# Optimization experiments

Hardware: AMD Instinct MI355X
Metric: run time of the kernel (lower is better)

The kernel has to match this reference:

```python
import jax, jax.numpy as jnp
import numpy as np

T, D, N, K, H = 4096, 2560, 8, 4, 256
QUERY_PRE_ATTN_SCALAR = 256.0
ROPE_THETA = 10000.0
RMS_EPS = 1e-6
SLIDING_WINDOW = 1024
NEG_INF = -1e30


def setup_inputs() -> dict:
    key = jax.random.key(0)
    ks = jax.random.split(key, 6)
    return {
        "x": jax.random.normal(ks[0], (T, D), dtype=jnp.float32),
        "wq": jax.random.normal(ks[1], (D, N, H), dtype=jnp.float32) * 0.02,
        "wk": jax.random.normal(ks[2], (D, K, H), dtype=jnp.float32) * 0.02,
        "wv": jax.random.normal(ks[3], (D, K, H), dtype=jnp.float32) * 0.02,
        "wo": jax.random.normal(ks[4], (N, H, D), dtype=jnp.float32) * 0.02,
        "q_norm_w": jnp.ones((H,), dtype=jnp.float32),
        "k_norm_w": jnp.ones((H,), dtype=jnp.float32),
        "positions": jnp.arange(T, dtype=jnp.int32),
    }


def rms_norm(x, w, eps=RMS_EPS):
    rms = jnp.sqrt(jnp.mean(x * x, axis=-1, keepdims=True) + eps)
    return w * (x / rms)


def apply_rope(x, positions, head_dim, theta):
    # x: [T, heads, H]; rotate-half RoPE
    half = head_dim // 2
    inv_freq = theta ** (-(jnp.arange(half, dtype=jnp.float32) * 2.0 / head_dim))
    ang = positions.astype(jnp.float32)[:, None] * inv_freq  # [T, half]
    sin = jnp.sin(ang)[:, None, :]
    cos = jnp.cos(ang)[:, None, :]
    x1, x2 = jnp.split(x, 2, axis=-1)
    return jnp.concatenate([x1 * cos - x2 * sin, x2 * cos + x1 * sin], axis=-1)


def reference(x, wq, wk, wv, wo, q_norm_w, k_norm_w, positions):
    # QKV projections (per-head)
    q = jnp.einsum('td,dnh->tnh', x, wq)            # [T, N, H]
    q = rms_norm(q, q_norm_w)
    q = q * (QUERY_PRE_ATTN_SCALAR ** -0.5)
    q = apply_rope(q, positions, H, ROPE_THETA)

    k = jnp.einsum('td,dkh->tkh', x, wk)            # [T, K, H]
    k = rms_norm(k, k_norm_w)
    k = apply_rope(k, positions, H, ROPE_THETA)

    v = jnp.einsum('td,dkh->tkh', x, wv)            # [T, K, H]

    # GQA sliding-window causal attention
    G = N // K
    qh = q.reshape(T, K, G, H)
    scores = jnp.einsum('tkgh,skh->kgts', qh, k)    # [K, G, T, T]
    pq = positions[:, None]
    pk = positions[None, :]
    mask = (pk <= pq) & (pq - pk < SLIDING_WINDOW)  # [T, T]
    scores = jnp.where(mask, scores, NEG_INF)
    p = jax.nn.softmax(scores, axis=-1)
    attn = jnp.einsum('kgts,skh->tkgh', p, v).reshape(T, N, H)

    o = jnp.einsum('tnh,nhd->td', attn, wo)         # [T, D]
    new_kv_cache = jnp.stack([k, v])                # [2, T, K, H]
    return new_kv_cache, o
```

## Files before the change

### kernel.cpp

```cpp
#include <hip/hip_runtime.h>
#include <stdint.h>

#define T_TOK 4096
#define DM    2560
#define NQ    8
#define NKV   4
#define HD    256
#define WIN   1024

using bf16x8 = __attribute__((ext_vector_type(8))) short;
using f32x4  = __attribute__((ext_vector_type(4))) float;
typedef unsigned short u16;

__device__ __forceinline__ u16 f2bf(float x) {
  union { float f; uint32_t u; } v; v.f = x;
  uint32_t u = v.u;
  return (u16)((u + 0x7fffu + ((u >> 16) & 1u)) >> 16);
}
__device__ __forceinline__ float bf2f(u16 b) {
  union { uint32_t u; float f; } v; v.u = ((uint32_t)b) << 16;
  return v.f;
}

__device__ __forceinline__ void async_cp16(const void* g, void* lds) {
  __builtin_amdgcn_global_load_lds(
      (const __attribute__((address_space(1))) uint32_t*)(uintptr_t)g,
      (__attribute__((address_space(3))) uint32_t*)(uint32_t)(uintptr_t)lds,
      16, 0, 0);
}

__global__ __launch_bounds__(256) void convert_f32_bf16(
    const float* __restrict__ in, u16* __restrict__ out, int n)
{
  for (int i = (blockIdx.x * 256 + threadIdx.x) * 4; i < n; i += gridDim.x * 256 * 4) {
    float4 v = *(const float4*)(in + i);
    ushort4 o;
    o.x = f2bf(v.x); o.y = f2bf(v.y); o.z = f2bf(v.z); o.w = f2bf(v.w);
    *(ushort4*)(out + i) = o;
  }
}

__global__ __launch_bounds__(256) void transpose_f32_bf16(
    const float* __restrict__ in, u16* __restrict__ out, int R, int C)
{
  __shared__ u16 tile[64][65];
  const int r0 = blockIdx.y * 64, c0 = blockIdx.x * 64;
  const int tr = threadIdx.x >> 6, tc = threadIdx.x & 63;
  #pragma unroll
  for (int i = 0; i < 16; ++i) {
    int r = tr + i * 4;
    tile[r][tc] = f2bf(in[(size_t)(r0 + r) * C + c0 + tc]);
  }
  __syncthreads();
  #pragma unroll
  for (int i = 0; i < 16; ++i) {
    int c = tr + i * 4;
    out[(size_t)(c0 + c) * R + r0 + tc] = tile[tc][c];
  }
}

template<bool F32OUT>
__global__ __launch_bounds__(512, 2) void gemm256(
    const u16* __restrict__ A, const u16* __restrict__ B, void* __restrict__ Cv,
    int Kd, int lda, int ldb, int ldc)
{
  __shared__ __align__(16) u16 lds[2][2][256 * 64];
  const int tid = threadIdx.x;
  const int wave = tid >> 6, lane = tid & 63;
  const int lg = lane >> 4, lc = lane & 15;
  const int wr = wave >> 2, wc = wave & 3;
  const int m0 = blockIdx.y * 256, n0 = blockIdx.x * 256;
  const int NT = Kd >> 6;

  const int srow = tid >> 3;
  const int scol = ((tid & 7) * 16) ^ ((srow & 7) << 4);
  const u16* Ag = A + (size_t)(m0 + srow) * lda + (scol >> 1);
  const u16* Bg = B + (size_t)(n0 + srow) * ldb + (scol >> 1);
  char* ldsA0 = (char*)&lds[0][0][0];
  char* ldsB0 = (char*)&lds[0][1][0];
  char* ldsA1 = (char*)&lds[1][0][0];
  char* ldsB1 = (char*)&lds[1][1][0];

  #define STAGE256(LA, LB, KT) do {                                         \
    const int kc_ = (KT) * 64;                                              \
    _Pragma("unroll")                                                       \
    for (int li = 0; li < 4; ++li)                                          \
      async_cp16(Ag + (size_t)(li * 64) * lda + kc_, (LA) + li * 8192 + wave * 1024); \
    _Pragma("unroll")                                                       \
    for (int li = 0; li < 4; ++li)                                          \
      async_cp16(Bg + (size_t)(li * 64) * ldb + kc_, (LB) + li * 8192 + wave * 1024); \
  } while (0)

  const f32x4 zf = {0.f, 0.f, 0.f, 0.f};
  f32x4 acc[8][4];
  #pragma unroll
  for (int i = 0; i < 8; ++i)
    #pragma unroll
    for (int j = 0; j < 4; ++j) acc[i][j] = zf;

  STAGE256(ldsA0, ldsB0, 0);
  STAGE256(ldsA1, ldsB1, 1);
  asm volatile("s_waitcnt vmcnt(8)" ::: "memory");
  __builtin_amdgcn_s_barrier();
  __builtin_amdgcn_sched_barrier(0);

  for (int t = 0; t < NT; ++t) {
    const int cur = t & 1;
    const u16* Ab = &lds[cur][0][0];
    const u16* Bb = &lds[cur][1][0];

    bf16x8 bf[4][2];
    #pragma unroll
    for (int j = 0; j < 4; ++j)
      #pragma unroll
      for (int k2 = 0; k2 < 2; ++k2) {
        const int row = wc * 64 + j * 16 + lc;
        const int cb = k2 * 64 + lg * 16;
        bf[j][k2] = *(const bf16x8*)((const char*)Bb + row * 128 + (cb ^ ((row & 7) << 4)));
      }

    #pragma unroll
    for (int p = 0; p < 4; ++p) {
      bf16x8 af[2][2];
      #pragma unroll
      for (int im = 0; im < 2; ++im)
        #pragma unroll
        for (int k2 = 0; k2 < 2; ++k2) {
          const int row = wr * 128 + (p * 2 + im) * 16 + lc;
          const int cb = k2 * 64 + lg * 16;
          af[im][k2] = *(const bf16x8*)((const char*)Ab + row * 128 + (cb ^ ((row & 7) << 4)));
        }
      __builtin_amdgcn_s_setprio(1);
      #pragma unroll
      for (int im = 0; im < 2; ++im)
        #pragma unroll
        for (int j = 0; j < 4; ++j)
          #pragma unroll
          for (int k2 = 0; k2 < 2; ++k2)
            acc[p * 2 + im][j] = __builtin_amdgcn_mfma_f32_16x16x32_bf16(
                af[im][k2], bf[j][k2], acc[p * 2 + im][j], 0, 0, 0);
      __builtin_amdgcn_s_setprio(0);
    }

    __builtin_amdgcn_s_barrier();
    __builtin_amdgcn_sched_barrier(0);
    int nk = t + 2; if (nk > NT - 1) nk = NT - 1;
    if (cur == 0) { STAGE256(ldsA0, ldsB0, nk); } else { STAGE256(ldsA1, ldsB1, nk); }
    asm volatile("s_waitcnt vmcnt(8)" ::: "memory");
    __builtin_amdgcn_s_barrier();
    __builtin_amdgcn_sched_barrier(0);
  }
  #undef STAGE256

  #pragma unroll
  for (int i = 0; i < 8; ++i)
    #pragma unroll
    for (int j = 0; j < 4; ++j)
      #pragma unroll
      for (int r = 0; r < 4; ++r) {
        const int row = m0 + wr * 128 + i * 16 + lg * 4 + r;
        const int col = n0 + wc * 64 + j * 16 + lc;
        if (F32OUT) ((float*)Cv)[(size_t)row * ldc + col] = acc[i][j][r];
        else        ((u16*)Cv)[(size_t)row * ldc + col] = f2bf(acc[i][j][r]);
      }
}

__global__ __launch_bounds__(256) void fuse_norm_rope(
    const u16* __restrict__ qkv, const float* __restrict__ qnw, const float* __restrict__ knw,
    const int* __restrict__ pos, u16* __restrict__ qb, u16* __restrict__ kb,
    u16* __restrict__ vb, float* __restrict__ kvout)
{
  const int t = blockIdx.x;
  const int wave = threadIdx.x >> 6, lane = threadIdx.x & 63;
  const float p = (float)pos[t];
  const float kf = 0.10381025296523007f;
  float s0, c0, s1, c1;
  sincosf(p * exp2f(-(float)lane * kf), &s0, &c0);
  sincosf(p * exp2f(-(float)(lane + 64) * kf), &s1, &c1);
  const u16* row = qkv + (size_t)t * 4096;

  for (int pp = 0; pp < 4; ++pp) {
    const int hr = pp * 4 + wave;
    if (hr >= 12) {
      const int kk = hr - 12;
      const u16* src = row + 3072 + kk * 256;
      float* dstf = kvout + (size_t)T_TOK * NKV * HD + ((size_t)t * NKV + kk) * HD;
      u16*   dstb = vb + ((size_t)t * NKV + kk) * HD;
      #pragma unroll
      for (int q4 = 0; q4 < 4; ++q4) {
        const u16 s = src[lane + q4 * 64];
        dstf[lane + q4 * 64] = bf2f(s);
        dstb[lane + q4 * 64] = s;
      }
    } else {
      const bool isq = hr < 8;
      const int cb = isq ? hr * 256 : 2048 + (hr - 8) * 256;
      float v0 = bf2f(row[cb + lane]);
      float v1 = bf2f(row[cb + lane + 64]);
      float v2 = bf2f(row[cb + lane + 128]);
      float v3 = bf2f(row[cb + lane + 192]);
      float ss = v0 * v0 + v1 * v1 + v2 * v2 + v3 * v3;
      #pragma unroll
      for (int off = 1; off < 64; off <<= 1) ss += __shfl_xor(ss, off);
      float sc = rsqrtf(ss * (1.0f / 256.0f) + 1e-6f);
      if (isq) sc *= 0.0625f;
      const float* wn = isq ? qnw : knw;
      v0 *= sc * wn[lane];
      v1 *= sc * wn[lane + 64];
      v2 *= sc * wn[lane + 128];
      v3 *= sc * wn[lane + 192];
      const float n0 = v0 * c0 - v2 * s0;
      const float n2 = v2 * c0 + v0 * s0;
      const float n1 = v1 * c1 - v3 * s1;
      const float n3 = v3 * c1 + v1 * s1;
      if (isq) {
        u16* dst = qb + (size_t)t * 2048 + hr * 256;
        dst[lane]       = f2bf(n0);
        dst[lane + 64]  = f2bf(n1);
        dst[lane + 128] = f2bf(n2);
        dst[lane + 192] = f2bf(n3);
      } else {
        const int kk = hr - 8;
        float* dstf = kvout + ((size_t)t * NKV + kk) * HD;
        dstf[lane]       = n0;
        dstf[lane + 64]  = n1;
        dstf[lane + 128] = n2;
        dstf[lane + 192] = n3;
        u16* dstb = kb + ((size_t)t * NKV + kk) * HD;
        dstb[lane]       = f2bf(n0);
        dstb[lane + 64]  = f2bf(n1);
        dstb[lane + 128] = f2bf(n2);
        dstb[lane + 192] = f2bf(n3);
      }
    }
  }
}

__global__ __launch_bounds__(256) void transpose_v(
    const u16* __restrict__ vc, u16* __restrict__ vt)
{
  __shared__ u16 tile[64][65];
  const int kk = blockIdx.z;
  const int t0 = blockIdx.y * 64, h0 = blockIdx.x * 64;
  const int tr = threadIdx.x >> 6, tc = threadIdx.x & 63;
  #pragma unroll
  for (int i = 0; i < 16; ++i) {
    int tt = tr + i * 4;
    tile[tt][tc] = vc[((size_t)(t0 + tt) * NKV + kk) * HD + h0 + tc];
  }
  __syncthreads();
  #pragma unroll
  for (int i = 0; i < 16; ++i) {
    int h = tr + i * 4;
    vt[(size_t)kk * HD * T_TOK + (size_t)(h0 + h) * T_TOK + t0 + tc] = tile[tc][h];
  }
}

__global__ __launch_bounds__(256, 2) void attn_kernel(
    const u16* __restrict__ qb, const u16* __restrict__ kc,
    const u16* __restrict__ vt, u16* __restrict__ ob)
{
  __shared__ __align__(16) u16 Ks[64 * 256];
  __shared__ __align__(16) u16 Vts[256 * 64];
  __shared__ __align__(16) u16 Ps[64 * 64];
  __shared__ float m_part[2][64], s_part[2][64];
  __shared__ float m_arr[64], l_arr[64], a_arr[64];

  const int n = blockIdx.y;
  const int kk = n >> 1;
  const int t0 = blockIdx.x * 64;
  const int tid = threadIdx.x;
  const int wave = tid >> 6, lane = tid & 63;
  const int lg = lane >> 4, lc = lane & 15;
  const int wr = wave >> 1, wc = wave & 1;
  const int lswz = (lc & 7) << 4;

  {
    const u16* qp = qb + (size_t)(t0 + (tid >> 5)) * 2048 + n * 256 + (tid & 31) * 8;
    u16* qd = Ks + (tid >> 5) * 256 + (tid & 31) * 8;
    bf16x8 tq[8];
    #pragma unroll
    for (int is = 0; is < 8; ++is) tq[is] = *(const bf16x8*)(qp + (size_t)is * 8 * 2048);
    #pragma unroll
    for (int is = 0; is < 8; ++is) *(bf16x8*)(qd + is * 8 * 256) = tq[is];
  }
  if (tid < 64) { m_arr[tid] = -1e30f; l_arr[tid] = 0.f; }
  __syncthreads();
  bf16x8 qf[8][2];
  #pragma unroll
  for (int ks = 0; ks < 8; ++ks)
    #pragma unroll
    for (int i = 0; i < 2; ++i)
      qf[ks][i] = *(const bf16x8*)&Ks[(wr * 32 + i * 16 + lc) * 256 + ks * 32 + lg * 8];
  __syncthreads();

  const f32x4 zf = {0.f, 0.f, 0.f, 0.f};
  f32x4 o_acc[2][8];
  #pragma unroll
  for (int i = 0; i < 2; ++i)
    #pragma unroll
    for (int j = 0; j < 8; ++j) o_acc[i][j] = zf;

  const int mtile = t0 >> 6;
  const int ktf = (mtile >= 16) ? (mtile - 16) : 0;
  for (int kt = ktf; kt <= mtile; ++kt) {
    const int kb = kt * 64;
    {
      bf16x8 t8[8];
      const u16* kp = kc + (size_t)(kb + (tid >> 5)) * (NKV * HD) + kk * HD + (tid & 31) * 8;
      #pragma unroll
      for (int is = 0; is < 8; ++is) t8[is] = *(const bf16x8*)(kp + (size_t)is * 8 * (NKV * HD));
      const int kswz = ((tid >> 5) & 7) << 4;
      #pragma unroll
      for (int is = 0; is < 8; ++is)
        *(bf16x8*)((char*)Ks + ((((tid >> 5) + is * 8) * 512 + (tid & 31) * 16) ^ kswz)) = t8[is];

      const u16* vp = vt + (size_t)kk * HD * T_TOK + (size_t)(tid >> 3) * T_TOK + kb + (tid & 7) * 8;
      #pragma unroll
      for (int is = 0; is < 8; ++is) t8[is] = *(const bf16x8*)(vp + (size_t)(is * 32) * T_TOK);
      const int vswz = ((tid >> 3) & 7) << 4;
      #pragma unroll
      for (int is = 0; is < 8; ++is)
        *(bf16x8*)((char*)Vts + ((((tid >> 3) + is * 32) * 128 + (tid & 7) * 16) ^ vswz)) = t8[is];
    }
    __syncthreads();

    f32x4 sf[2][2];
    #pragma unroll
    for (int i = 0; i < 2; ++i) { sf[i][0] = zf; sf[i][1] = zf; }
    #pragma unroll
    for (int ks = 0; ks < 8; ++ks) {
      bf16x8 kf0 = *(const bf16x8*)((char*)Ks + (((wc * 32 + lc) * 512 + ks * 64 + lg * 16) ^ lswz));
      bf16x8 kf1 = *(const bf16x8*)((char*)Ks + (((wc * 32 + 16 + lc) * 512 + ks * 64 + lg * 16) ^ lswz));
      sf[0][0] = __builtin_amdgcn_mfma_f32_16x16x32_bf16(qf[ks][0], kf0, sf[0][0], 0, 0, 0);
      sf[0][1] = __builtin_amdgcn_mfma_f32_16x16x32_bf16(qf[ks][0], kf1, sf[0][1], 0, 0, 0);
      sf[1][0] = __builtin_amdgcn_mfma_f32_16x16x32_bf16(qf[ks][1], kf0, sf[1][0], 0, 0, 0);
      sf[1][1] = __builtin_amdgcn_mfma_f32_16x16x32_bf16(qf[ks][1], kf1, sf[1][1], 0, 0, 0);
    }

    const bool interior = (kb >= t0 - 960) && (kb <= t0 - 64);
    if (!interior) {
      #pragma unroll
      for (int i = 0; i < 2; ++i)
        #pragma unroll
        for (int jj = 0; jj < 2; ++jj) {
          const int gcol = kb + wc * 32 + jj * 16 + lc;
          #pragma unroll
          for (int r = 0; r < 4; ++r) {
            const int grow = t0 + wr * 32 + i * 16 + lg * 4 + r;
            if ((unsigned)(grow - gcol) >= WIN) sf[i][jj][r] = -1e30f;
          }
        }
    }

    #pragma unroll
    for (int i = 0; i < 2; ++i) {
      float v0 = fmaxf(sf[i][0][0], sf[i][1][0]);
      float v1 = fmaxf(sf[i][0][1], sf[i][1][1]);
      float v2 = fmaxf(sf[i][0][2], sf[i][1][2]);
      float v3 = fmaxf(sf[i][0][3], sf[i][1][3]);
      #pragma unroll
      for (int off = 1; off < 16; off <<= 1) {
        v0 = fmaxf(v0, __shfl_xor(v0, off));
        v1 = fmaxf(v1, __shfl_xor(v1, off));
        v2 = fmaxf(v2, __shfl_xor(v2, off));
        v3 = fmaxf(v3, __shfl_xor(v3, off));
      }
      if (lc == 0) {
        const int rb = wr * 32 + i * 16 + lg * 4;
        m_part[wc][rb + 0] = v0;
        m_part[wc][rb + 1] = v1;
        m_part[wc][rb + 2] = v2;
        m_part[wc][rb + 3] = v3;
      }
    }
    __syncthreads();
    if (tid < 64) {
      const float tm = fmaxf(m_part[0][tid], m_part[1][tid]);
      const float mo = m_arr[tid];
      const float mn = fmaxf(mo, tm);
      m_arr[tid] = mn;
      a_arr[tid] = __expf(mo - mn);
    }
    __syncthreads();

    #pragma unroll
    for (int i = 0; i < 2; ++i) {
      float su0 = 0.f, su1 = 0.f, su2 = 0.f, su3 = 0.f;
      #pragma unroll
      for (int r = 0; r < 4; ++r) {
        const int row = wr * 32 + i * 16 + lg * 4 + r;
        const float m = m_arr[row];
        const float p0 = __expf(sf[i][0][r] - m);
        const float p1 = __expf(sf[i][1][r] - m);
        const int rswz = (row & 7) << 4;
        *(u16*)((char*)Ps + ((row * 128 + (wc * 32 + lc) * 2) ^ rswz))      = f2bf(p0);
        *(u16*)((char*)Ps + ((row * 128 + (wc * 32 + 16 + lc) * 2) ^ rswz)) = f2bf(p1);
        const float s = p0 + p1;
        if (r == 0) su0 = s; else if (r == 1) su1 = s; else if (r == 2) su2 = s; else su3 = s;
      }
      #pragma unroll
      for (int off = 1; off < 16; off <<= 1) {
        su0 += __shfl_xor(su0, off);
        su1 += __shfl_xor(su1, off);
        su2 += __shfl_xor(su2, off);
        su3 += __shfl_xor(su3, off);
      }
      if (lc == 0) {
        const int rb = wr * 32 + i * 16 + lg * 4;
        s_part[wc][rb + 0] = su0;
        s_part[wc][rb + 1] = su1;
        s_part[wc][rb + 2] = su2;
        s_part[wc][rb + 3] = su3;
      }
    }
    #pragma unroll
    for (int i = 0; i < 2; ++i) {
      const int rb = wr * 32 + i * 16 + lg * 4;
      const float a0 = a_arr[rb + 0], a1 = a_arr[rb + 1], a2 = a_arr[rb + 2], a3 = a_arr[rb + 3];
      #pragma unroll
      for (int j = 0; j < 8; ++j) {
        o_acc[i][j][0] *= a0;
        o_acc[i][j][1] *= a1;
        o_acc[i][j][2] *= a2;
        o_acc[i][j][3] *= a3;
      }
    }
    __syncthreads();
    if (tid < 64)
      l_arr[tid] = l_arr[tid] * a_arr[tid] + (s_part[0][tid] + s_part[1][tid]);

    #pragma unroll
    for (int ks = 0; ks < 2; ++ks) {
      bf16x8 pa0 = *(const bf16x8*)((char*)Ps + (((wr * 32 + lc) * 128 + ks * 64 + lg * 16) ^ lswz));
      bf16x8 pa1 = *(const bf16x8*)((char*)Ps + (((wr * 32 + 16 + lc) * 128 + ks * 64 + lg * 16) ^ lswz));
      #pragma unroll
      for (int j = 0; j < 8; ++j) {
        bf16x8 vf = *(const bf16x8*)((char*)Vts + (((wc * 128 + j * 16 + lc) * 128 + ks * 64 + lg * 16) ^ lswz));
        o_acc[0][j] = __builtin_amdgcn_mfma_f32_16x16x32_bf16(pa0, vf, o_acc[0][j], 0, 0, 0);
        o_acc[1][j] = __builtin_amdgcn_mfma_f32_16x16x32_bf16(pa1, vf, o_acc[1][j], 0, 0, 0);
      }
    }
    __syncthreads();
  }

  #pragma unroll
  for (int i = 0; i < 2; ++i) {
    const int rb = wr * 32 + i * 16 + lg * 4;
    const float li0 = 1.f / l_arr[rb + 0];
    const float li1 = 1.f / l_arr[rb + 1];
    const float li2 = 1.f / l_arr[rb + 2];
    const float li3 = 1.f / l_arr[rb + 3];
    #pragma unroll
    for (int j = 0; j < 8; ++j) {
      const int colb = n * 256 + wc * 128 + j * 16 + lc;
      ob[(size_t)(t0 + rb + 0) * 2048 + colb] = f2bf(o_acc[i][j][0] * li0);
      ob[(size_t)(t0 + rb + 1) * 2048 + colb] = f2bf(o_acc[i][j][1] * li1);
      ob[(size_t)(t0 + rb + 2) * 2048 + colb] = f2bf(o_acc[i][j][2] * li2);
      ob[(size_t)(t0 + rb + 3) * 2048 + colb] = f2bf(o_acc[i][j][3] * li3);
    }
  }
}

extern "C" void kernel_launch(void* const* d_in, const int* in_sizes, int n_in,
                              void* d_out, int out_size, void* d_ws, size_t ws_size,
                              hipStream_t stream)
{
  (void)in_sizes; (void)n_in; (void)out_size; (void)ws_size;
  const float* x   = (const float*)d_in[0];
  const float* wq  = (const float*)d_in[1];
  const float* wk  = (const float*)d_in[2];
  const float* wv  = (const float*)d_in[3];
  const float* wo  = (const float*)d_in[4];
  const float* qnw = (const float*)d_in[5];
  const float* knw = (const float*)d_in[6];
  const int*   pos = (const int*)d_in[7];
  float* out = (float*)d_out;

  char* ws = (char*)d_ws;
  u16* woT   = (u16*)(ws);
  u16* xb    = (u16*)(ws + 10485760);
  u16* wqkvT = (u16*)(ws + 31457280);
  u16* qkv   = (u16*)(ws + 52428800);
  u16* q_b   = xb;
  u16* kb    = wqkvT;
  u16* vb    = (u16*)(ws + 31457280 + 8388608);
  u16* vtb   = qkv;
  u16* attn  = (u16*)(ws + 52428800 + 8388608);

  convert_f32_bf16<<<2048, 256, 0, stream>>>(x, xb, T_TOK * DM);
  transpose_f32_bf16<<<dim3(32, 40), 256, 0, stream>>>(wq, wqkvT, DM, 2048);
  transpose_f32_bf16<<<dim3(16, 40), 256, 0, stream>>>(wk, wqkvT + 2048 * DM, DM, 1024);
  transpose_f32_bf16<<<dim3(16, 40), 256, 0, stream>>>(wv, wqkvT + 3072 * DM, DM, 1024);
  transpose_f32_bf16<<<dim3(40, 32), 256, 0, stream>>>(wo, woT, 2048, DM);

  gemm256<false><<<dim3(16, 16), 512, 0, stream>>>(xb, wqkvT, qkv, DM, DM, DM, 4096);

  fuse_norm_rope<<<T_TOK, 256, 0, stream>>>(qkv, qnw, knw, pos, q_b, kb, vb, out);

  transpose_v<<<dim3(4, 64, 4), 256, 0, stream>>>(vb, vtb);

  attn_kernel<<<dim3(64, 8), 256, 0, stream>>>(q_b, kb, vtb, attn);

  gemm256<true><<<dim3(10, 16), 512, 0, stream>>>(attn, woT, out + 2 * (size_t)T_TOK * NKV * HD,
                                                  2048, 2048, 2048, DM);
}
```

Measured before the change: 286.9 us.

## Restructure attention per-wave softmax with register prefetch and remap GEMM blocks

The attention kernel now gives each wave 16 full query rows across all 64 keys. This keeps softmax max, sum and rescale state in registers and drops the shared-memory reductions and most block barriers. The next K/V tile is prefetched into registers while the current one is computed, and MFMA sections raise wave priority. The GEMMs switch to a 1D grid with a swizzled block-to-tile mapping meant to improve L2 locality across XCDs. The cost is higher register pressure (16 output accumulators per lane plus prefetch buffers), which may reduce occupancy.

```diff
diff --git a/kernel.cpp b/kernel.cpp
--- a/kernel.cpp
+++ b/kernel.cpp
@@ -69,7 +69,9 @@
   const int wave = tid >> 6, lane = tid & 63;
   const int lg = lane >> 4, lc = lane & 15;
   const int wr = wave >> 2, wc = wave & 3;
-  const int m0 = blockIdx.y * 256, n0 = blockIdx.x * 256;
+  const int nwg = gridDim.x, bid = blockIdx.x;
+  const int nid = (bid & 7) * (nwg >> 3) + (bid >> 3);
+  const int m0 = (nid & 15) * 256, n0 = (nid >> 4) * 256;
   const int NT = Kd >> 6;
 
   const int srow = tid >> 3;
@@ -262,203 +264,162 @@
 {
   __shared__ __align__(16) u16 Ks[64 * 256];
   __shared__ __align__(16) u16 Vts[256 * 64];
-  __shared__ __align__(16) u16 Ps[64 * 64];
-  __shared__ float m_part[2][64], s_part[2][64];
-  __shared__ float m_arr[64], l_arr[64], a_arr[64];
-
-  const int n = blockIdx.y;
-  const int kk = n >> 1;
+  __shared__ __align__(16) u16 Ps[4][16 * 64];
+
+  const int n = blockIdx.y, kk = n >> 1;
   const int t0 = blockIdx.x * 64;
   const int tid = threadIdx.x;
   const int wave = tid >> 6, lane = tid & 63;
   const int lg = lane >> 4, lc = lane & 15;
-  const int wr = wave >> 1, wc = wave & 1;
   const int lswz = (lc & 7) << 4;
-
+  const f32x4 zf = {0.f, 0.f, 0.f, 0.f};
+
+  bf16x8 qf[8];
   {
-    const u16* qp = qb + (size_t)(t0 + (tid >> 5)) * 2048 + n * 256 + (tid & 31) * 8;
-    u16* qd = Ks + (tid >> 5) * 256 + (tid & 31) * 8;
-    bf16x8 tq[8];
-    #pragma unroll
-    for (int is = 0; is < 8; ++is) tq[is] = *(const bf16x8*)(qp + (size_t)is * 8 * 2048);
-    #pragma unroll
-    for (int is = 0; is < 8; ++is) *(bf16x8*)(qd + is * 8 * 256) = tq[is];
-  }
-  if (tid < 64) { m_arr[tid] = -1e30f; l_arr[tid] = 0.f; }
-  __syncthreads();
-  bf16x8 qf[8][2];
-  #pragma unroll
-  for (int ks = 0; ks < 8; ++ks)
-    #pragma unroll
-    for (int i = 0; i < 2; ++i)
-      qf[ks][i] = *(const bf16x8*)&Ks[(wr * 32 + i * 16 + lc) * 256 + ks * 32 + lg * 8];
-  __syncthreads();
-
-  const f32x4 zf = {0.f, 0.f, 0.f, 0.f};
-  f32x4 o_acc[2][8];
-  #pragma unroll
-  for (int i = 0; i < 2; ++i)
-    #pragma unroll
-    for (int j = 0; j < 8; ++j) o_acc[i][j] = zf;
+    const u16* qp = qb + (size_t)(t0 + wave * 16 + lc) * 2048 + n * 256 + lg * 8;
+    #pragma unroll
+    for (int ks = 0; ks < 8; ++ks) qf[ks] = *(const bf16x8*)(qp + ks * 32);
+  }
+
+  f32x4 o_acc[16];
+  #pragma unroll
+  for (int j = 0; j < 16; ++j) o_acc[j] = zf;
+  float m_r[4], l_r[4];
+  #pragma unroll
+  for (int r = 0; r < 4; ++r) { m_r[r] = -1e30f; l_r[r] = 0.f; }
 
   const int mtile = t0 >> 6;
   const int ktf = (mtile >= 16) ? (mtile - 16) : 0;
+
+  const int krow = tid >> 5;
+  const int kcol = (tid & 31) * 8;
+  const int kswz = (krow & 7) << 4;
+  const int vrow = tid >> 3;
+  const int vcol = (tid & 7) * 8;
+  const int vswz = (vrow & 7) << 4;
+
+  bf16x8 rk[8], rv[8];
+  {
+    const int kb = ktf * 64;
+    const u16* kp = kc + (size_t)(kb + krow) * (NKV * HD) + kk * HD + kcol;
+    const u16* vp = vt + (size_t)kk * (HD * T_TOK) + (size_t)vrow * T_TOK + kb + vcol;
+    #pragma unroll
+    for (int is = 0; is < 8; ++is) rk[is] = *(const bf16x8*)(kp + (size_t)(is * 8) * (NKV * HD));
+    #pragma unroll
+    for (int is = 0; is < 8; ++is) rv[is] = *(const bf16x8*)(vp + (size_t)(is * 32) * T_TOK);
+  }
+
   for (int kt = ktf; kt <= mtile; ++kt) {
     const int kb = kt * 64;
-    {
-      bf16x8 t8[8];
-      const u16* kp = kc + (size_t)(kb + (tid >> 5)) * (NKV * HD) + kk * HD + (tid & 31) * 8;
-      #pragma unroll
-      for (int is = 0; is < 8; ++is) t8[is] = *(const bf16x8*)(kp + (size_t)is * 8 * (NKV * HD));
-      const int kswz = ((tid >> 5) & 7) << 4;
-      #pragma unroll
-      for (int is = 0; is < 8; ++is)
-        *(bf16x8*)((char*)Ks + ((((tid >> 5) + is * 8) * 512 + (tid & 31) * 16) ^ kswz)) = t8[is];
-
-      const u16* vp = vt + (size_t)kk * HD * T_TOK + (size_t)(tid >> 3) * T_TOK + kb + (tid & 7) * 8;
-      #pragma unroll
-      for (int is = 0; is < 8; ++is) t8[is] = *(const bf16x8*)(vp + (size_t)(is * 32) * T_TOK);
-      const int vswz = ((tid >> 3) & 7) << 4;
-      #pragma unroll
-      for (int is = 0; is < 8; ++is)
-        *(bf16x8*)((char*)Vts + ((((tid >> 3) + is * 32) * 128 + (tid & 7) * 16) ^ vswz)) = t8[is];
-    }
+    #pragma unroll
+    for (int is = 0; is < 8; ++is)
+      *(bf16x8*)((char*)Ks + (((krow + is * 8) * 512 + kcol * 2) ^ kswz)) = rk[is];
+    #pragma unroll
+    for (int is = 0; is < 8; ++is)
+      *(bf16x8*)((char*)Vts + (((vrow + is * 32) * 128 + vcol * 2) ^ vswz)) = rv[is];
     __syncthreads();
 
-    f32x4 sf[2][2];
-    #pragma unroll
-    for (int i = 0; i < 2; ++i) { sf[i][0] = zf; sf[i][1] = zf; }
-    #pragma unroll
-    for (int ks = 0; ks < 8; ++ks) {
-      bf16x8 kf0 = *(const bf16x8*)((char*)Ks + (((wc * 32 + lc) * 512 + ks * 64 + lg * 16) ^ lswz));
-      bf16x8 kf1 = *(const bf16x8*)((char*)Ks + (((wc * 32 + 16 + lc) * 512 + ks * 64 + lg * 16) ^ lswz));
-      sf[0][0] = __builtin_amdgcn_mfma_f32_16x16x32_bf16(qf[ks][0], kf0, sf[0][0], 0, 0, 0);
-      sf[0][1] = __builtin_amdgcn_mfma_f32_16x16x32_bf16(qf[ks][0], kf1, sf[0][1], 0, 0, 0);
-      sf[1][0] = __builtin_amdgcn_mfma_f32_16x16x32_bf16(qf[ks][1], kf0, sf[1][0], 0, 0, 0);
-      sf[1][1] = __builtin_amdgcn_mfma_f32_16x16x32_bf16(qf[ks][1], kf1, sf[1][1], 0, 0, 0);
-    }
+    if (kt < mtile) {
+      const int nb = kb + 64;
+      const u16* kp = kc + (size_t)(nb + krow) * (NKV * HD) + kk * HD + kcol;
+      const u16* vp = vt + (size_t)kk * (HD * T_TOK) + (size_t)vrow * T_TOK + nb + vcol;
+      #pragma unroll
+      for (int is = 0; is < 8; ++is) rk[is] = *(const bf16x8*)(kp + (size_t)(is * 8) * (NKV * HD));
+      #pragma unroll
+      for (int is = 0; is < 8; ++is) rv[is] = *(const bf16x8*)(vp + (size_t)(is * 32) * T_TOK);
+    }
+
+    f32x4 sf[4];
+    #pragma unroll
+    for (int j = 0; j < 4; ++j) sf[j] = zf;
+    __builtin_amdgcn_s_setprio(1);
+    #pragma unroll
+    for (int ks = 0; ks < 8; ++ks)
+      #pragma unroll
+      for (int j = 0; j < 4; ++j) {
+        const int row = j * 16 + lc;
+        bf16x8 kf = *(const bf16x8*)((char*)Ks + ((row * 512 + ks * 64 + lg * 16) ^ lswz));
+        sf[j] = __builtin_amdgcn_mfma_f32_16x16x32_bf16(qf[ks], kf, sf[j], 0, 0, 0);
+      }
+    __builtin_amdgcn_s_setprio(0);
 
     const bool interior = (kb >= t0 - 960) && (kb <= t0 - 64);
     if (!interior) {
       #pragma unroll
-      for (int i = 0; i < 2; ++i)
+      for (int j = 0; j < 4; ++j) {
+        const int gcol = kb + j * 16 + lc;
         #pragma unroll
-        for (int jj = 0; jj < 2; ++jj) {
-          const int gcol = kb + wc * 32 + jj * 16 + lc;
-          #pragma unroll
-          for (int r = 0; r < 4; ++r) {
-            const int grow = t0 + wr * 32 + i * 16 + lg * 4 + r;
-            if ((unsigned)(grow - gcol) >= WIN) sf[i][jj][r] = -1e30f;
-          }
+        for (int r = 0; r < 4; ++r) {
+          const int grow = t0 + wave * 16 + lg * 4 + r;
+          if ((unsigned)(grow - gcol) >= WIN) sf[j][r] = -1e30f;
         }
-    }
-
-    #pragma unroll
-    for (int i = 0; i < 2; ++i) {
-      float v0 = fmaxf(sf[i][0][0], sf[i][1][0]);
-      float v1 = fmaxf(sf[i][0][1], sf[i][1][1]);
-      float v2 = fmaxf(sf[i][0][2], sf[i][1][2]);
-      float v3 = fmaxf(sf[i][0][3], sf[i][1][3]);
-      #pragma unroll
-      for (int off = 1; off < 16; off <<= 1) {
-        v0 = fmaxf(v0, __shfl_xor(v0, off));
-        v1 = fmaxf(v1, __shfl_xor(v1, off));
-        v2 = fmaxf(v2, __shfl_xor(v2, off));
-        v3 = fmaxf(v3, __shfl_xor(v3, off));
-      }
-      if (lc == 0) {
-        const int rb = wr * 32 + i * 16 + lg * 4;
-        m_part[wc][rb + 0] = v0;
-        m_part[wc][rb + 1] = v1;
-        m_part[wc][rb + 2] = v2;
-        m_part[wc][rb + 3] = v3;
-      }
-    }
+      }
+    }
+
+    float a_r[4];
+    #pragma unroll
+    for (int r = 0; r < 4; ++r) {
+      float v = fmaxf(fmaxf(sf[0][r], sf[1][r]), fmaxf(sf[2][r], sf[3][r]));
+      v = fmaxf(v, __shfl_xor(v, 1));
+      v = fmaxf(v, __shfl_xor(v, 2));
+      v = fmaxf(v, __shfl_xor(v, 4));
+      v = fmaxf(v, __shfl_xor(v, 8));
+      const float mn = fmaxf(m_r[r], v);
+      a_r[r] = __expf(m_r[r] - mn);
+      m_r[r] = mn;
+    }
+
+    char* myP = (char*)&Ps[wave][0];
+    #pragma unroll
+    for (int r = 0; r < 4; ++r) {
+      const int row = lg * 4 + r;
+      const int rsw = (row & 7) << 4;
+      float su = 0.f;
+      #pragma unroll
+      for (int j = 0; j < 4; ++j) {
+        const float p = __expf(sf[j][r] - m_r[r]);
+        su += p;
+        *(u16*)(myP + ((row * 128 + (j * 16 + lc) * 2) ^ rsw)) = f2bf(p);
+      }
+      su += __shfl_xor(su, 1);
+      su += __shfl_xor(su, 2);
+      su += __shfl_xor(su, 4);
+      su += __shfl_xor(su, 8);
+      l_r[r] = l_r[r] * a_r[r] + su;
+    }
+
+    #pragma unroll
+    for (int j = 0; j < 16; ++j) {
+      o_acc[j][0] *= a_r[0];
+      o_acc[j][1] *= a_r[1];
+      o_acc[j][2] *= a_r[2];
+      o_acc[j][3] *= a_r[3];
+    }
+
+    bf16x8 pa[2];
+    #pragma unroll
+    for (int ks = 0; ks < 2; ++ks)
+      pa[ks] = *(const bf16x8*)(myP + ((lc * 128 + ks * 64 + lg * 16) ^ lswz));
+    __builtin_amdgcn_s_setprio(1);
+    #pragma unroll
+    for (int ks = 0; ks < 2; ++ks)
+      #pragma unroll
+      for (int j = 0; j < 16; ++j) {
+        const int row = j * 16 + lc;
+        bf16x8 vf = *(const bf16x8*)((char*)Vts + ((row * 128 + ks * 64 + lg * 16) ^ lswz));
+        o_acc[j] = __builtin_amdgcn_mfma_f32_16x16x32_bf16(pa[ks], vf, o_acc[j], 0, 0, 0);
+      }
+    __builtin_amdgcn_s_setprio(0);
     __syncthreads();
-    if (tid < 64) {
-      const float tm = fmaxf(m_part[0][tid], m_part[1][tid]);
-      const float mo = m_arr[tid];
-      const float mn = fmaxf(mo, tm);
-      m_arr[tid] = mn;
-      a_arr[tid] = __expf(mo - mn);
-    }
-    __syncthreads();
-
-    #pragma unroll
-    for (int i = 0; i < 2; ++i) {
-      float su0 = 0.f, su1 = 0.f, su2 = 0.f, su3 = 0.f;
-      #pragma unroll
-      for (int r = 0; r < 4; ++r) {
-        const int row = wr * 32 + i * 16 + lg * 4 + r;
-        const float m = m_arr[row];
-        const float p0 = __expf(sf[i][0][r] - m);
-        const float p1 = __expf(sf[i][1][r] - m);
-        const int rswz = (row & 7) << 4;
-        *(u16*)((char*)Ps + ((row * 128 + (wc * 32 + lc) * 2) ^ rswz))      = f2bf(p0);
-        *(u16*)((char*)Ps + ((row * 128 + (wc * 32 + 16 + lc) * 2) ^ rswz)) = f2bf(p1);
-        const float s = p0 + p1;
-        if (r == 0) su0 = s; else if (r == 1) su1 = s; else if (r == 2) su2 = s; else su3 = s;
-      }
-      #pragma unroll
-      for (int off = 1; off < 16; off <<= 1) {
-        su0 += __shfl_xor(su0, off);
-        su1 += __shfl_xor(su1, off);
-        su2 += __shfl_xor(su2, off);
-        su3 += __shfl_xor(su3, off);
-      }
-      if (lc == 0) {
-        const int rb = wr * 32 + i * 16 + lg * 4;
-        s_part[wc][rb + 0] = su0;
-        s_part[wc][rb + 1] = su1;
-        s_part[wc][rb + 2] = su2;
-        s_part[wc][rb + 3] = su3;
-      }
-    }
-    #pragma unroll
-    for (int i = 0; i < 2; ++i) {
-      const int rb = wr * 32 + i * 16 + lg * 4;
-      const float a0 = a_arr[rb + 0], a1 = a_arr[rb + 1], a2 = a_arr[rb + 2], a3 = a_arr[rb + 3];
-      #pragma unroll
-      for (int j = 0; j < 8; ++j) {
-        o_acc[i][j][0] *= a0;
-        o_acc[i][j][1] *= a1;
-        o_acc[i][j][2] *= a2;
-        o_acc[i][j][3] *= a3;
-      }
-    }
-    __syncthreads();
-    if (tid < 64)
-      l_arr[tid] = l_arr[tid] * a_arr[tid] + (s_part[0][tid] + s_part[1][tid]);
-
-    #pragma unroll
-    for (int ks = 0; ks < 2; ++ks) {
-      bf16x8 pa0 = *(const bf16x8*)((char*)Ps + (((wr * 32 + lc) * 128 + ks * 64 + lg * 16) ^ lswz));
-      bf16x8 pa1 = *(const bf16x8*)((char*)Ps + (((wr * 32 + 16 + lc) * 128 + ks * 64 + lg * 16) ^ lswz));
-      #pragma unroll
-      for (int j = 0; j < 8; ++j) {
-        bf16x8 vf = *(const bf16x8*)((char*)Vts + (((wc * 128 + j * 16 + lc) * 128 + ks * 64 + lg * 16) ^ lswz));
-        o_acc[0][j] = __builtin_amdgcn_mfma_f32_16x16x32_bf16(pa0, vf, o_acc[0][j], 0, 0, 0);
-        o_acc[1][j] = __builtin_amdgcn_mfma_f32_16x16x32_bf16(pa1, vf, o_acc[1][j], 0, 0, 0);
-      }
-    }
-    __syncthreads();
-  }
-
-  #pragma unroll
-  for (int i = 0; i < 2; ++i) {
-    const int rb = wr * 32 + i * 16 + lg * 4;
-    const float li0 = 1.f / l_arr[rb + 0];
-    const float li1 = 1.f / l_arr[rb + 1];
-    const float li2 = 1.f / l_arr[rb + 2];
-    const float li3 = 1.f / l_arr[rb + 3];
-    #pragma unroll
-    for (int j = 0; j < 8; ++j) {
-      const int colb = n * 256 + wc * 128 + j * 16 + lc;
-      ob[(size_t)(t0 + rb + 0) * 2048 + colb] = f2bf(o_acc[i][j][0] * li0);
-      ob[(size_t)(t0 + rb + 1) * 2048 + colb] = f2bf(o_acc[i][j][1] * li1);
-      ob[(size_t)(t0 + rb + 2) * 2048 + colb] = f2bf(o_acc[i][j][2] * li2);
-      ob[(size_t)(t0 + rb + 3) * 2048 + colb] = f2bf(o_acc[i][j][3] * li3);
-    }
+  }
+
+  #pragma unroll
+  for (int r = 0; r < 4; ++r) {
+    const float li = 1.f / l_r[r];
+    const size_t rowb = (size_t)(t0 + wave * 16 + lg * 4 + r) * 2048 + n * 256 + lc;
+    #pragma unroll
+    for (int j = 0; j < 16; ++j)
+      ob[rowb + j * 16] = f2bf(o_acc[j][r] * li);
   }
 }
 
@@ -494,7 +455,7 @@
   transpose_f32_bf16<<<dim3(16, 40), 256, 0, stream>>>(wv, wqkvT + 3072 * DM, DM, 1024);
   transpose_f32_bf16<<<dim3(40, 32), 256, 0, stream>>>(wo, woT, 2048, DM);
 
-  gemm256<false><<<dim3(16, 16), 512, 0, stream>>>(xb, wqkvT, qkv, DM, DM, DM, 4096);
+  gemm256<false><<<256, 512, 0, stream>>>(xb, wqkvT, qkv, DM, DM, DM, 4096);
 
   fuse_norm_rope<<<T_TOK, 256, 0, stream>>>(qkv, qnw, knw, pos, q_b, kb, vb, out);
 
@@ -502,6 +463,6 @@
 
   attn_kernel<<<dim3(64, 8), 256, 0, stream>>>(q_b, kb, vtb, attn);
 
-  gemm256<true><<<dim3(10, 16), 512, 0, stream>>>(attn, woT, out + 2 * (size_t)T_TOK * NKV * HD,
-                                                  2048, 2048, 2048, DM);
-}
+  gemm256<true><<<160, 512, 0, stream>>>(attn, woT, out + 2 * (size_t)T_TOK * NKV * HD,
+                                         2048, 2048, 2048, DM);
+}
```

New measurement: 462.2 us. 61.1% more time.
